# Performance work log

Measured on AMD Instinct MI355X. Metric: run time of the kernel, lower is better.

Reference implementation:

```python
import jax, jax.numpy as jnp
import numpy as np

N, E, HID, HEADS, KHOPS = 10000, 160000, 64, 8, 3
D = HID // HEADS  # head_dim = 8


def setup_inputs() -> dict:
    key = jax.random.key(0)
    ks = jax.random.split(key, 8)
    s = 1.0 / np.sqrt(HID)
    return {
        "x": jax.random.normal(ks[0], (N, HID), jnp.float32),
        "edge_index": jax.random.randint(ks[1], (2, E), 0, N),
        "edge_feature": jax.random.normal(ks[2], (E, HID), jnp.float32),
        "edge_weight": jax.random.uniform(ks[3], (E,), jnp.float32),
        "Wq": jax.random.normal(ks[4], (HID, HID), jnp.float32) * s,
        "bq": jnp.zeros((HID,), jnp.float32),
        "Wk": jax.random.normal(ks[5], (HID, HID), jnp.float32) * s,
        "bk": jnp.zeros((HID,), jnp.float32),
        "Wv": jax.random.normal(ks[6], (HID, HID), jnp.float32) * s,
        "bv": jnp.zeros((HID,), jnp.float32),
        "hopwise": jnp.ones((KHOPS + 1,), jnp.float32),
    }


def reference(x, edge_index, edge_feature, edge_weight, Wq, bq, Wk, bk, Wv, bv, hopwise):
    n = x.shape[0]
    row, col = edge_index[0], edge_index[1]

    # symmetric degree normalization, scaled by edge_weight
    deg = jax.ops.segment_sum(jnp.ones_like(edge_weight), col, num_segments=n)
    deg_inv = jnp.where(deg > 0, deg ** -0.5, 0.0)
    norm = deg_inv[row] * deg_inv[col] * edge_weight  # [E]

    Q = jax.nn.relu(x @ Wq + bq).reshape(n, HEADS, D)
    K = (x @ Wk + bk).reshape(n, HEADS, D)
    V = (x @ Wv + bv).reshape(n, HEADS, D)
    ef = edge_feature.reshape(-1, HEADS, D)  # [E,h,d]

    hidden = V * hopwise[0]
    sqrt_d = jnp.sqrt(jnp.asarray(D, x.dtype))

    for hop in range(KHOPS):
        if hop == 0:
            Kj = jax.nn.relu(K[row] + ef)                 # [E,h,d]
            # per-edge K (x) V outer product message, scatter-summed at col
            msg = norm[:, None, None, None] * jnp.einsum('ehi,ehj->ehij', Kj, V[row])
            M = jax.ops.segment_sum(msg, col, num_segments=n)   # [N,h,d,d]
            K = jax.ops.segment_sum(norm[:, None, None] * Kj, col, num_segments=n)
        else:
            M = jax.ops.segment_sum(norm[:, None, None, None] * M[row], col, num_segments=n)
            K = jax.ops.segment_sum(norm[:, None, None] * K[row], col, num_segments=n)

        H = jnp.einsum('nhi,nhij->nhj', Q, M)             # [N,h,d]
        nrm = jnp.sqrt(jnp.sum((H / sqrt_d) ** 2, axis=-1))  # [N,h]
        H = H / jnp.maximum(jnp.ones_like(nrm), nrm)[..., None]
        hidden = hidden + hopwise[hop + 1] * H

    return hidden.reshape(n, HEADS * D)
```

## Files before the change

kernel.cpp:

```cpp
#include <hip/hip_runtime.h>
#include <hip/hip_bf16.h>


#define HIDC 64
#define MELEMS 512

__device__ __forceinline__ unsigned bf16rne(float x) {
    unsigned u = __float_as_uint(x);
    return (u + 0x7FFFu + ((u >> 16) & 1u)) >> 16;
}
__device__ __forceinline__ unsigned pack2(float lo, float hi) {
    return bf16rne(lo) | (bf16rne(hi) << 16);
}
__device__ __forceinline__ float bfval(unsigned short v) {
    return __uint_as_float((unsigned)v << 16);
}
__device__ __forceinline__ void acc8(float* acc, float s, uint4 a) {
    acc[0] = fmaf(s, __uint_as_float(a.x << 16), acc[0]);
    acc[1] = fmaf(s, __uint_as_float(a.x & 0xFFFF0000u), acc[1]);
    acc[2] = fmaf(s, __uint_as_float(a.y << 16), acc[2]);
    acc[3] = fmaf(s, __uint_as_float(a.y & 0xFFFF0000u), acc[3]);
    acc[4] = fmaf(s, __uint_as_float(a.z << 16), acc[4]);
    acc[5] = fmaf(s, __uint_as_float(a.z & 0xFFFF0000u), acc[5]);
    acc[6] = fmaf(s, __uint_as_float(a.w << 16), acc[6]);
    acc[7] = fmaf(s, __uint_as_float(a.w & 0xFFFF0000u), acc[7]);
}

__global__ __launch_bounds__(256) void qkv_kernel(
    const float* __restrict__ x,
    const float* __restrict__ Wq, const float* __restrict__ bq,
    const float* __restrict__ Wk, const float* __restrict__ bk,
    const float* __restrict__ Wv, const float* __restrict__ bv,
    const float* __restrict__ hopwise,
    float* __restrict__ Q, float* __restrict__ K, float* __restrict__ V,
    float* __restrict__ out, int* __restrict__ deg,
    int* __restrict__ counter, int n) {
    int gid = blockIdx.x * blockDim.x + threadIdx.x;
    if (gid < n) deg[gid] = 0;
    if (gid == 0) *counter = 0;
    int c = gid & 63;
    int nb = (gid >> 6) * 4;
    if (nb >= n) return;
    int mcnt = min(4, n - nb);
    float aq[4], ak[4], av[4];
    #pragma unroll
    for (int m = 0; m < 4; ++m) { aq[m] = bq[c]; ak[m] = bk[c]; av[m] = bv[c]; }
    const float4* x4 = (const float4*)x;
    for (int k4 = 0; k4 < 16; ++k4) {
        float4 xv[4];
        #pragma unroll
        for (int m = 0; m < 4; ++m)
            xv[m] = x4[(size_t)(nb + (m < mcnt ? m : 0)) * 16 + k4];
        #pragma unroll
        for (int kk = 0; kk < 4; ++kk) {
            int k = k4 * 4 + kk;
            float wq = Wq[k * HIDC + c], wk = Wk[k * HIDC + c], wv = Wv[k * HIDC + c];
            #pragma unroll
            for (int m = 0; m < 4; ++m) {
                float xvk = (kk == 0) ? xv[m].x : (kk == 1) ? xv[m].y
                          : (kk == 2) ? xv[m].z : xv[m].w;
                aq[m] = fmaf(xvk, wq, aq[m]);
                ak[m] = fmaf(xvk, wk, ak[m]);
                av[m] = fmaf(xvk, wv, av[m]);
            }
        }
    }
    #pragma unroll
    for (int m = 0; m < 4; ++m) {
        if (m < mcnt) {
            size_t idx = (size_t)(nb + m) * HIDC + c;
            Q[idx] = fmaxf(aq[m], 0.f);
            K[idx] = ak[m];
            V[idx] = av[m];
            out[idx] = hopwise[0] * av[m];
        }
    }
}

__global__ void deg_kernel(const int* __restrict__ col, int* __restrict__ deg, int e) {
    int i = blockIdx.x * blockDim.x + threadIdx.x;
    if (i < e) atomicAdd(&deg[col[i]], 1);
}

__global__ __launch_bounds__(1024) void base_kernel(const int* __restrict__ deg,
                                                    int* __restrict__ counter,
                                                    int* __restrict__ rowbeg,
                                                    int* __restrict__ cursor, int n) {
    __shared__ int wsum[16];
    __shared__ int blockbase;
    int i = blockIdx.x * 1024 + threadIdx.x;
    int lane = threadIdx.x & 63, w = threadIdx.x >> 6;
    int v = (i < n) ? deg[i] : 0;
    int s = v;
    #pragma unroll
    for (int off = 1; off < 64; off <<= 1) {
        int t = __shfl_up(s, off);
        if (lane >= off) s += t;
    }
    if (lane == 63) wsum[w] = s;
    __syncthreads();
    if (threadIdx.x == 0) {
        int acc = 0;
        #pragma unroll
        for (int w2 = 0; w2 < 16; ++w2) { int t = wsum[w2]; wsum[w2] = acc; acc += t; }
        blockbase = atomicAdd(counter, acc);
    }
    __syncthreads();
    int excl = blockbase + wsum[w] + s - v;
    if (i < n) {
        rowbeg[i] = excl;
        cursor[i] = excl;
    }
}

__global__ __launch_bounds__(256) void stage_kernel(
    const int* __restrict__ row, const int* __restrict__ col,
    const float* __restrict__ ew, const int* __restrict__ deg,
    int* __restrict__ cursor, int* __restrict__ srcrow,
    float* __restrict__ snorm,
    const float* __restrict__ K, const float* __restrict__ V,
    const float* __restrict__ ef, unsigned short* __restrict__ kjv, int e) {
    int gtid = blockIdx.x * blockDim.x + threadIdx.x;
    int i = gtid >> 4;
    if (i >= e) return;
    int c4 = gtid & 15;
    int lane = threadIdx.x & 63;
    int lb = lane & 48;
    int r = 0, pos = 0;
    if (c4 == 0) {
        r = row[i];
        int cc = col[i];
        int dr = deg[r], dc = deg[cc];
        float nv = ew[i];
        nv *= (dr > 0) ? rsqrtf((float)dr) : 0.f;
        nv *= (dc > 0) ? rsqrtf((float)dc) : 0.f;
        pos = atomicAdd(&cursor[cc], 1);
        srcrow[pos] = r;
        snorm[pos] = nv;
    }
    r = __shfl(r, lb);
    pos = __shfl(pos, lb);
    const float4* efv = (const float4*)ef;
    const float4* Kv = (const float4*)K;
    const float4* Vv = (const float4*)V;
    float4 f = efv[(size_t)i * 16 + c4];
    float4 kk = Kv[(size_t)r * 16 + c4];
    float4 vv = Vv[(size_t)r * 16 + c4];
    uint2 kjp, vp;
    kjp.x = pack2(fmaxf(kk.x + f.x, 0.f), fmaxf(kk.y + f.y, 0.f));
    kjp.y = pack2(fmaxf(kk.z + f.z, 0.f), fmaxf(kk.w + f.w, 0.f));
    vp.x = pack2(vv.x, vv.y);
    vp.y = pack2(vv.z, vv.w);
    uint2* rowp = (uint2*)(kjv + (size_t)pos * 128);
    rowp[c4] = kjp;
    rowp[16 + c4] = vp;
}

__device__ __forceinline__ void epilogue64(const float* acc, const float* __restrict__ Q,
                                           float hw, int n, int h, int ii,
                                           float* __restrict__ out) {
    float q = Q[n * HIDC + h * 8 + ii];
    float p[8];
    #pragma unroll
    for (int j = 0; j < 8; ++j) p[j] = q * acc[j];
    #pragma unroll
    for (int off = 1; off < 8; off <<= 1) {
        #pragma unroll
        for (int j = 0; j < 8; ++j) p[j] += __shfl_xor(p[j], off);
    }
    float ssq = 0.f;
    #pragma unroll
    for (int j = 0; j < 8; ++j) ssq = fmaf(p[j], p[j], ssq);
    float nr = sqrtf(ssq * 0.125f);
    float sc = (nr > 1.f) ? (hw / nr) : hw;
    if (ii == 0) {
        float4* o = (float4*)(out + (size_t)n * HIDC + h * 8);
        float4 c0 = o[0], c1 = o[1];
        c0.x = fmaf(p[0], sc, c0.x); c0.y = fmaf(p[1], sc, c0.y);
        c0.z = fmaf(p[2], sc, c0.z); c0.w = fmaf(p[3], sc, c0.w);
        c1.x = fmaf(p[4], sc, c1.x); c1.y = fmaf(p[5], sc, c1.y);
        c1.z = fmaf(p[6], sc, c1.z); c1.w = fmaf(p[7], sc, c1.w);
        o[0] = c0; o[1] = c1;
    }
}

__global__ __launch_bounds__(256) void hop0_kernel(
    const int* __restrict__ rowbeg, const int* __restrict__ deg,
    const float* __restrict__ snorm, const unsigned short* __restrict__ kjv,
    const float* __restrict__ Q, const float* __restrict__ hopwise,
    unsigned short* __restrict__ M0, float* __restrict__ out, int nn) {
    int n = blockIdx.x * 4 + (threadIdx.x >> 6);
    if (n >= nn) return;
    int t = threadIdx.x & 63;
    int h = t >> 3, ii = t & 7;
    int beg = rowbeg[n], end = beg + deg[n];
    float acc[8] = {0, 0, 0, 0, 0, 0, 0, 0};
    int k = beg;
    for (; k + 4 <= end; k += 4) {
        float s0 = snorm[k]     * bfval(kjv[(size_t)(k)     * 128 + t]);
        float s1 = snorm[k + 1] * bfval(kjv[(size_t)(k + 1) * 128 + t]);
        float s2 = snorm[k + 2] * bfval(kjv[(size_t)(k + 2) * 128 + t]);
        float s3 = snorm[k + 3] * bfval(kjv[(size_t)(k + 3) * 128 + t]);
        uint4 v0 = *(const uint4*)(kjv + (size_t)(k)     * 128 + 64 + h * 8);
        uint4 v1 = *(const uint4*)(kjv + (size_t)(k + 1) * 128 + 64 + h * 8);
        uint4 v2 = *(const uint4*)(kjv + (size_t)(k + 2) * 128 + 64 + h * 8);
        uint4 v3 = *(const uint4*)(kjv + (size_t)(k + 3) * 128 + 64 + h * 8);
        acc8(acc, s0, v0);
        acc8(acc, s1, v1);
        acc8(acc, s2, v2);
        acc8(acc, s3, v3);
    }
    for (; k < end; ++k) {
        float s = snorm[k] * bfval(kjv[(size_t)k * 128 + t]);
        uint4 v = *(const uint4*)(kjv + (size_t)k * 128 + 64 + h * 8);
        acc8(acc, s, v);
    }
    uint4 st;
    st.x = pack2(acc[0], acc[1]); st.y = pack2(acc[2], acc[3]);
    st.z = pack2(acc[4], acc[5]); st.w = pack2(acc[6], acc[7]);
    ((uint4*)M0)[(size_t)n * 64 + t] = st;
    epilogue64(acc, Q, hopwise[1], n, h, ii, out);
}

__global__ __launch_bounds__(256) void hopk_kernel(
    const int* __restrict__ rowbeg, const int* __restrict__ deg,
    const int* __restrict__ srcrow, const float* __restrict__ snorm,
    const unsigned short* __restrict__ Min, const float* __restrict__ Q,
    const float* __restrict__ hopwise, int hopidx,
    unsigned short* __restrict__ Mout, int writeM, float* __restrict__ out, int nn) {
    int n = blockIdx.x * 4 + (threadIdx.x >> 6);
    if (n >= nn) return;
    int t = threadIdx.x & 63;
    int beg = rowbeg[n], end = beg + deg[n];
    float acc[8] = {0, 0, 0, 0, 0, 0, 0, 0};
    const uint4* Mv = (const uint4*)Min;
    int k = beg;
    for (; k + 8 <= end; k += 8) {
        int j0 = srcrow[k],     j1 = srcrow[k + 1], j2 = srcrow[k + 2], j3 = srcrow[k + 3];
        int j4 = srcrow[k + 4], j5 = srcrow[k + 5], j6 = srcrow[k + 6], j7 = srcrow[k + 7];
        uint4 a0 = Mv[(size_t)j0 * 64 + t];
        uint4 a1 = Mv[(size_t)j1 * 64 + t];
        uint4 a2 = Mv[(size_t)j2 * 64 + t];
        uint4 a3 = Mv[(size_t)j3 * 64 + t];
        uint4 a4 = Mv[(size_t)j4 * 64 + t];
        uint4 a5 = Mv[(size_t)j5 * 64 + t];
        uint4 a6 = Mv[(size_t)j6 * 64 + t];
        uint4 a7 = Mv[(size_t)j7 * 64 + t];
        acc8(acc, snorm[k],     a0);
        acc8(acc, snorm[k + 1], a1);
        acc8(acc, snorm[k + 2], a2);
        acc8(acc, snorm[k + 3], a3);
        acc8(acc, snorm[k + 4], a4);
        acc8(acc, snorm[k + 5], a5);
        acc8(acc, snorm[k + 6], a6);
        acc8(acc, snorm[k + 7], a7);
    }
    for (; k + 4 <= end; k += 4) {
        int j0 = srcrow[k], j1 = srcrow[k + 1], j2 = srcrow[k + 2], j3 = srcrow[k + 3];
        uint4 a0 = Mv[(size_t)j0 * 64 + t];
        uint4 a1 = Mv[(size_t)j1 * 64 + t];
        uint4 a2 = Mv[(size_t)j2 * 64 + t];
        uint4 a3 = Mv[(size_t)j3 * 64 + t];
        acc8(acc, snorm[k],     a0);
        acc8(acc, snorm[k + 1], a1);
        acc8(acc, snorm[k + 2], a2);
        acc8(acc, snorm[k + 3], a3);
    }
    for (; k < end; ++k) acc8(acc, snorm[k], Mv[(size_t)srcrow[k] * 64 + t]);
    if (writeM) {
        uint4 st;
        st.x = pack2(acc[0], acc[1]); st.y = pack2(acc[2], acc[3]);
        st.z = pack2(acc[4], acc[5]); st.w = pack2(acc[6], acc[7]);
        ((uint4*)Mout)[(size_t)n * 64 + t] = st;
    }
    int h = t >> 3, ii = t & 7;
    epilogue64(acc, Q, hopwise[hopidx], n, h, ii, out);
}

extern "C" void kernel_launch(void* const* d_in, const int* in_sizes, int n_in,
                              void* d_out, int out_size, void* d_ws, size_t ws_size,
                              hipStream_t stream) {
    const float* x       = (const float*)d_in[0];
    const int*   ei      = (const int*)d_in[1];
    const float* ef      = (const float*)d_in[2];
    const float* ew      = (const float*)d_in[3];
    const float* Wq      = (const float*)d_in[4];
    const float* bq      = (const float*)d_in[5];
    const float* Wk      = (const float*)d_in[6];
    const float* bk      = (const float*)d_in[7];
    const float* Wv      = (const float*)d_in[8];
    const float* bv      = (const float*)d_in[9];
    const float* hopwise = (const float*)d_in[10];
    float* out = (float*)d_out;

    const int n = in_sizes[0] / HIDC;
    const int e = in_sizes[1] / 2;
    const int* row = ei;
    const int* col = ei + e;

    char* base = (char*)d_ws;
    size_t off = 0;
    auto alloc = [&](size_t bytes) -> void* {
        void* p = base + off;
        off = (off + bytes + 255) & ~(size_t)255;
        return p;
    };
    int*            deg     = (int*)           alloc((size_t)n * 4);
    int*            cursor  = (int*)           alloc((size_t)n * 4);
    int*            rowbeg  = (int*)           alloc((size_t)n * 4);
    int*            counter = (int*)           alloc(256);
    int*            srcrow  = (int*)           alloc((size_t)e * 4);
    float*          snorm   = (float*)         alloc((size_t)e * 4);
    unsigned short* kjv     = (unsigned short*)alloc((size_t)e * 128 * 2);
    float*          Q       = (float*)         alloc((size_t)n * HIDC * 4);
    float*          K       = (float*)         alloc((size_t)n * HIDC * 4);
    float*          V       = (float*)         alloc((size_t)n * HIDC * 4);
    unsigned short* M0      = (unsigned short*)alloc((size_t)n * MELEMS * 2);
    unsigned short* M1      = (unsigned short*)alloc((size_t)n * MELEMS * 2);
    (void)ws_size;

    int qthreads = ((n + 3) / 4) * 64;
    int qb = (qthreads + 255) / 256;
    qkv_kernel<<<qb, 256, 0, stream>>>(x, Wq, bq, Wk, bk, Wv, bv, hopwise,
                                       Q, K, V, out, deg, counter, n);

    int eb = (e + 255) / 256;
    deg_kernel<<<eb, 256, 0, stream>>>(col, deg, e);

    int bb = (n + 1023) / 1024;
    base_kernel<<<bb, 1024, 0, stream>>>(deg, counter, rowbeg, cursor, n);

    int sb = ((e * 16) + 255) / 256;
    stage_kernel<<<sb, 256, 0, stream>>>(row, col, ew, deg, cursor,
                                         srcrow, snorm, K, V, ef, kjv, e);

    int nb = (n + 3) / 4;
    hop0_kernel<<<nb, 256, 0, stream>>>(rowbeg, deg, snorm, kjv, Q, hopwise, M0, out, n);
    hopk_kernel<<<nb, 256, 0, stream>>>(rowbeg, deg, srcrow, snorm, M0, Q, hopwise, 2, M1, 1, out, n);
    hopk_kernel<<<nb, 256, 0, stream>>>(rowbeg, deg, srcrow, snorm, M1, Q, hopwise, 3, M0, 0, out, n);
}
```

Before: 127.6 us.

## Gather bf16 V by source row in hop0 instead of staging per-edge V copies

The stage kernel stops writing a per-edge bf16 copy of V and instead stores only the norm-scaled relu(K+ef) row (64 bf16 per edge). The QKV kernel writes V directly as bf16, and hop0 gathers V from the source node through srcrow. This halves the per-edge staging buffer and cuts the write and re-read traffic in stage and hop0, at the price of random gathers from a small V table that should mostly stay cached. Folding the norm into the stored Kj removes a multiply per edge in hop0 but rounds nv*Kj to bf16 as one product.

After: 122.4 us. 4.1% less time.

```diff
diff --git a/kernel.cpp b/kernel.cpp
--- a/kernel.cpp
+++ b/kernel.cpp
@@ -32,7 +32,8 @@
     const float* __restrict__ Wk, const float* __restrict__ bk,
     const float* __restrict__ Wv, const float* __restrict__ bv,
     const float* __restrict__ hopwise,
-    float* __restrict__ Q, float* __restrict__ K, float* __restrict__ V,
+    float* __restrict__ Q, float* __restrict__ K,
+    unsigned short* __restrict__ Vb,
     float* __restrict__ out, int* __restrict__ deg,
     int* __restrict__ counter, int n) {
     int gid = blockIdx.x * blockDim.x + threadIdx.x;
@@ -71,7 +72,7 @@
             size_t idx = (size_t)(nb + m) * HIDC + c;
             Q[idx] = fmaxf(aq[m], 0.f);
             K[idx] = ak[m];
-            V[idx] = av[m];
+            Vb[idx] = (unsigned short)bf16rne(av[m]);
             out[idx] = hopwise[0] * av[m];
         }
     }
@@ -118,8 +119,8 @@
     const float* __restrict__ ew, const int* __restrict__ deg,
     int* __restrict__ cursor, int* __restrict__ srcrow,
     float* __restrict__ snorm,
-    const float* __restrict__ K, const float* __restrict__ V,
-    const float* __restrict__ ef, unsigned short* __restrict__ kjv, int e) {
+    const float* __restrict__ K, const float* __restrict__ ef,
+    unsigned short* __restrict__ kjn, int e) {
     int gtid = blockIdx.x * blockDim.x + threadIdx.x;
     int i = gtid >> 4;
     if (i >= e) return;
@@ -127,11 +128,12 @@
     int lane = threadIdx.x & 63;
     int lb = lane & 48;
     int r = 0, pos = 0;
+    float nv = 0.f;
     if (c4 == 0) {
         r = row[i];
         int cc = col[i];
         int dr = deg[r], dc = deg[cc];
-        float nv = ew[i];
+        nv = ew[i];
         nv *= (dr > 0) ? rsqrtf((float)dr) : 0.f;
         nv *= (dc > 0) ? rsqrtf((float)dc) : 0.f;
         pos = atomicAdd(&cursor[cc], 1);
@@ -140,20 +142,15 @@
     }
     r = __shfl(r, lb);
     pos = __shfl(pos, lb);
+    nv = __shfl(nv, lb);
     const float4* efv = (const float4*)ef;
     const float4* Kv = (const float4*)K;
-    const float4* Vv = (const float4*)V;
     float4 f = efv[(size_t)i * 16 + c4];
     float4 kk = Kv[(size_t)r * 16 + c4];
-    float4 vv = Vv[(size_t)r * 16 + c4];
-    uint2 kjp, vp;
-    kjp.x = pack2(fmaxf(kk.x + f.x, 0.f), fmaxf(kk.y + f.y, 0.f));
-    kjp.y = pack2(fmaxf(kk.z + f.z, 0.f), fmaxf(kk.w + f.w, 0.f));
-    vp.x = pack2(vv.x, vv.y);
-    vp.y = pack2(vv.z, vv.w);
-    uint2* rowp = (uint2*)(kjv + (size_t)pos * 128);
-    rowp[c4] = kjp;
-    rowp[16 + c4] = vp;
+    uint2 kjp;
+    kjp.x = pack2(nv * fmaxf(kk.x + f.x, 0.f), nv * fmaxf(kk.y + f.y, 0.f));
+    kjp.y = pack2(nv * fmaxf(kk.z + f.z, 0.f), nv * fmaxf(kk.w + f.w, 0.f));
+    ((uint2*)(kjn + (size_t)pos * 64))[c4] = kjp;
 }
 
 __device__ __forceinline__ void epilogue64(const float* acc, const float* __restrict__ Q,
@@ -186,7 +183,8 @@
 
 __global__ __launch_bounds__(256) void hop0_kernel(
     const int* __restrict__ rowbeg, const int* __restrict__ deg,
-    const float* __restrict__ snorm, const unsigned short* __restrict__ kjv,
+    const int* __restrict__ srcrow, const unsigned short* __restrict__ kjn,
+    const unsigned short* __restrict__ Vb,
     const float* __restrict__ Q, const float* __restrict__ hopwise,
     unsigned short* __restrict__ M0, float* __restrict__ out, int nn) {
     int n = blockIdx.x * 4 + (threadIdx.x >> 6);
@@ -197,22 +195,24 @@
     float acc[8] = {0, 0, 0, 0, 0, 0, 0, 0};
     int k = beg;
     for (; k + 4 <= end; k += 4) {
-        float s0 = snorm[k]     * bfval(kjv[(size_t)(k)     * 128 + t]);
-        float s1 = snorm[k + 1] * bfval(kjv[(size_t)(k + 1) * 128 + t]);
-        float s2 = snorm[k + 2] * bfval(kjv[(size_t)(k + 2) * 128 + t]);
-        float s3 = snorm[k + 3] * bfval(kjv[(size_t)(k + 3) * 128 + t]);
-        uint4 v0 = *(const uint4*)(kjv + (size_t)(k)     * 128 + 64 + h * 8);
-        uint4 v1 = *(const uint4*)(kjv + (size_t)(k + 1) * 128 + 64 + h * 8);
-        uint4 v2 = *(const uint4*)(kjv + (size_t)(k + 2) * 128 + 64 + h * 8);
-        uint4 v3 = *(const uint4*)(kjv + (size_t)(k + 3) * 128 + 64 + h * 8);
+        int j0 = srcrow[k],     j1 = srcrow[k + 1];
+        int j2 = srcrow[k + 2], j3 = srcrow[k + 3];
+        float s0 = bfval(kjn[(size_t)(k)     * 64 + t]);
+        float s1 = bfval(kjn[(size_t)(k + 1) * 64 + t]);
+        float s2 = bfval(kjn[(size_t)(k + 2) * 64 + t]);
+        float s3 = bfval(kjn[(size_t)(k + 3) * 64 + t]);
+        uint4 v0 = *(const uint4*)(Vb + (size_t)j0 * 64 + h * 8);
+        uint4 v1 = *(const uint4*)(Vb + (size_t)j1 * 64 + h * 8);
+        uint4 v2 = *(const uint4*)(Vb + (size_t)j2 * 64 + h * 8);
+        uint4 v3 = *(const uint4*)(Vb + (size_t)j3 * 64 + h * 8);
         acc8(acc, s0, v0);
         acc8(acc, s1, v1);
         acc8(acc, s2, v2);
         acc8(acc, s3, v3);
     }
     for (; k < end; ++k) {
-        float s = snorm[k] * bfval(kjv[(size_t)k * 128 + t]);
-        uint4 v = *(const uint4*)(kjv + (size_t)k * 128 + 64 + h * 8);
+        float s = bfval(kjn[(size_t)k * 64 + t]);
+        uint4 v = *(const uint4*)(Vb + (size_t)srcrow[k] * 64 + h * 8);
         acc8(acc, s, v);
     }
     uint4 st;
@@ -311,10 +311,10 @@
     int*            counter = (int*)           alloc(256);
     int*            srcrow  = (int*)           alloc((size_t)e * 4);
     float*          snorm   = (float*)         alloc((size_t)e * 4);
-    unsigned short* kjv     = (unsigned short*)alloc((size_t)e * 128 * 2);
+    unsigned short* kjn     = (unsigned short*)alloc((size_t)e * HIDC * 2);
     float*          Q       = (float*)         alloc((size_t)n * HIDC * 4);
     float*          K       = (float*)         alloc((size_t)n * HIDC * 4);
-    float*          V       = (float*)         alloc((size_t)n * HIDC * 4);
+    unsigned short* Vb      = (unsigned short*)alloc((size_t)n * HIDC * 2);
     unsigned short* M0      = (unsigned short*)alloc((size_t)n * MELEMS * 2);
     unsigned short* M1      = (unsigned short*)alloc((size_t)n * MELEMS * 2);
     (void)ws_size;
@@ -322,7 +322,7 @@
     int qthreads = ((n + 3) / 4) * 64;
     int qb = (qthreads + 255) / 256;
     qkv_kernel<<<qb, 256, 0, stream>>>(x, Wq, bq, Wk, bk, Wv, bv, hopwise,
-                                       Q, K, V, out, deg, counter, n);
+                                       Q, K, Vb, out, deg, counter, n);
 
     int eb = (e + 255) / 256;
     deg_kernel<<<eb, 256, 0, stream>>>(col, deg, e);
@@ -332,10 +332,11 @@
 
     int sb = ((e * 16) + 255) / 256;
     stage_kernel<<<sb, 256, 0, stream>>>(row, col, ew, deg, cursor,
-                                         srcrow, snorm, K, V, ef, kjv, e);
+                                         srcrow, snorm, K, ef, kjn, e);
 
     int nb = (n + 3) / 4;
-    hop0_kernel<<<nb, 256, 0, stream>>>(rowbeg, deg, snorm, kjv, Q, hopwise, M0, out, n);
+    hop0_kernel<<<nb, 256, 0, stream>>>(rowbeg, deg, srcrow, kjn, Vb, Q,
+                                        hopwise, M0, out, n);
     hopk_kernel<<<nb, 256, 0, stream>>>(rowbeg, deg, srcrow, snorm, M0, Q, hopwise, 2, M1, 1, out, n);
     hopk_kernel<<<nb, 256, 0, stream>>>(rowbeg, deg, srcrow, snorm, M1, Q, hopwise, 3, M0, 0, out, n);
 }
```
